# Kernel tuning notes

Hardware: AMD Instinct MI355X
Metric: run time of the kernel (lower is better)

## Reference

```python
import jax, jax.numpy as jnp
import numpy as np

HEADS = 4


def _forward(x_atoms, pos, edge_attr, molecular_features, emb_W, emb_b, mp_W1, mp_b1, mp_W2, mp_b2, ln_g, ln_b, attn_in_w, attn_in_b, attn_out_w, attn_out_b, pool_W, pool_b, mol_gate, lrn_gate, molemb_W1, molemb_b1, molemb_W2, molemb_b2, lrnemb_W1, lrnemb_b1, lrnemb_W2, lrnemb_b2, fus_W1, fus_b1, fus_W2, fus_b2, head_W1, head_b1, head_W2, head_b2, edge_index, batch_idx):
    N = x_atoms.shape[0]
    B = molecular_features.shape[0]
    A = N // B  # equal-size molecules; batch_idx = repeat(arange(B), A)
    H = emb_W.shape[1]
    L = mp_W1.shape[0]
    src, dst = edge_index[0], edge_index[1]  # PyG: x_j = x[src], x_i = x[dst]
    x = x_atoms @ emb_W + emb_b
    # distance features (constant across layers)
    diff = pos[dst] - pos[src]
    d = jnp.sqrt(jnp.sum(diff * diff, axis=1, keepdims=True) + 1e-12)
    dist_feat = jnp.concatenate([d, 1.0 / (1.0 + d), jnp.exp(-d)], axis=1)  # [E,3]
    ones_e = jnp.ones((src.shape[0], 1), x.dtype)
    cnt = jnp.maximum(jax.ops.segment_sum(ones_e, dst, num_segments=N), 1.0)
    for l in range(L):
        res = x
        msg = jnp.concatenate([x[dst], x[src], dist_feat], axis=1)  # [E, 2H+3]
        msg = jax.nn.relu(msg @ mp_W1[l] + mp_b1[l]) @ mp_W2[l] + mp_b2[l]
        x = jax.ops.segment_sum(msg, dst, num_segments=N) / cnt  # mean aggregation
        y = x + res
        mu = y.mean(-1, keepdims=True)
        var = jnp.var(y, axis=-1, keepdims=True)
        x = (y - mu) * jax.lax.rsqrt(var + 1e-5) * ln_g[l] + ln_b[l]
    xm = x.reshape(B, A, H)
    explicit = xm.mean(axis=1)  # scatter_mean over equal-size graphs
    # per-molecule multi-head self-attention (torch MHA, eval mode)
    hd = H // HEADS
    qkv = xm @ attn_in_w.T + attn_in_b
    q, k, v = jnp.split(qkv, 3, axis=-1)
    q = q.reshape(B, A, HEADS, hd)
    k = k.reshape(B, A, HEADS, hd)
    v = v.reshape(B, A, HEADS, hd)
    scores = jnp.einsum('bqhd,bkhd->bhqk', q, k) / jnp.sqrt(jnp.asarray(hd, x.dtype))
    att = jax.nn.softmax(scores, axis=-1)
    o = jnp.einsum('bhqk,bkhd->bqhd', att, v).reshape(B, A, H)
    attended = o @ attn_out_w.T + attn_out_b
    aw = jax.nn.softmax(jnp.sum(attended * xm, axis=-1), axis=1)  # [B,A]
    wmean = jnp.sum(attended * aw[..., None], axis=1)
    maxp = attended.max(axis=1)
    meanp = attended.mean(axis=1)
    stdp = jnp.std(attended, axis=1, ddof=1)  # torch.std unbiased
    pooled = jnp.stack([wmean, maxp, meanp, stdp], axis=0)  # [4,B,H]
    proj = jnp.einsum('kbh,khf->kbf', pooled, pool_W) + pool_b[:, None, :]
    learned = jnp.moveaxis(proj, 0, 1).reshape(B, -1)  # [B,LF]
    # per-property gated MLPs, vectorized over P (atom gates are computed but unused in the source)
    gm = molecular_features[None] * jax.nn.sigmoid(mol_gate)[:, None, :]
    gl = learned[None] * jax.nn.sigmoid(lrn_gate)[:, None, :]
    molrep = jax.nn.relu(jnp.einsum('pbm,pmh->pbh', gm, molemb_W1) + molemb_b1[:, None, :])
    molrep = jnp.einsum('pbh,phk->pbk', molrep, molemb_W2) + molemb_b2[:, None, :]
    lrnrep = jax.nn.relu(jnp.einsum('pbm,pmh->pbh', gl, lrnemb_W1) + lrnemb_b1[:, None, :])
    lrnrep = jnp.einsum('pbh,phk->pbk', lrnrep, lrnemb_W2) + lrnemb_b2[:, None, :]
    P = mol_gate.shape[0]
    comb = jnp.concatenate([jnp.broadcast_to(explicit[None], (P, B, H)), molrep, lrnrep], axis=-1)
    fused = jax.nn.relu(jnp.einsum('pbc,pch->pbh', comb, fus_W1) + fus_b1[:, None, :])
    fused = jnp.einsum('pbh,phk->pbk', fused, fus_W2) + fus_b2[:, None, :]
    h = jax.nn.relu(jnp.einsum('pbh,phk->pbk', fused, head_W1) + head_b1[:, None, :])
    out = jnp.einsum('pbk,pko->pbo', h, head_W2) + head_b2[:, None, :]
    return out  # [P,B,1]: stacked predictions for the 4 properties


def setup_inputs() -> dict:
    key = jax.random.key(0)
    ks = jax.random.split(key, 24)
    B, A, F, M, H, LF, L, P = 1024, 32, 64, 200, 128, 64, 3, 4
    N = B * A
    E = N * 16
    H2, H4, Q = H // 2, H // 4, LF // 4
    n = lambda i, shape, s=1.0: jax.random.normal(ks[i], shape, dtype=jnp.float32) * s
    inp = {}
    inp['x_atoms'] = n(0, (N, F))
    inp['pos'] = n(1, (N, 3)) * 3.0
    inp['edge_attr'] = n(2, (E, 4))
    inp['molecular_features'] = n(3, (B, M))
    inp['emb_W'] = n(4, (F, H), 0.1)
    inp['emb_b'] = jnp.zeros((H,), jnp.float32)
    inp['mp_W1'] = n(5, (L, 2 * H + 3, H), 0.05)
    inp['mp_b1'] = jnp.zeros((L, H), jnp.float32)
    inp['mp_W2'] = n(6, (L, H, H), 0.05)
    inp['mp_b2'] = jnp.zeros((L, H), jnp.float32)
    inp['ln_g'] = jnp.ones((L, H), jnp.float32)
    inp['ln_b'] = jnp.zeros((L, H), jnp.float32)
    inp['attn_in_w'] = n(7, (3 * H, H), 0.08)
    inp['attn_in_b'] = jnp.zeros((3 * H,), jnp.float32)
    inp['attn_out_w'] = n(8, (H, H), 0.08)
    inp['attn_out_b'] = jnp.zeros((H,), jnp.float32)
    inp['pool_W'] = n(9, (4, H, Q), 0.08)
    inp['pool_b'] = jnp.zeros((4, Q), jnp.float32)
    inp['mol_gate'] = n(10, (P, M))
    inp['lrn_gate'] = n(11, (P, LF))
    inp['molemb_W1'] = n(12, (P, M, H2), 0.08)
    inp['molemb_b1'] = jnp.zeros((P, H2), jnp.float32)
    inp['molemb_W2'] = n(13, (P, H2, H2), 0.08)
    inp['molemb_b2'] = jnp.zeros((P, H2), jnp.float32)
    inp['lrnemb_W1'] = n(14, (P, LF, H2), 0.08)
    inp['lrnemb_b1'] = jnp.zeros((P, H2), jnp.float32)
    inp['lrnemb_W2'] = n(15, (P, H2, H2), 0.08)
    inp['lrnemb_b2'] = jnp.zeros((P, H2), jnp.float32)
    inp['fus_W1'] = n(16, (P, 2 * H, H), 0.08)
    inp['fus_b1'] = jnp.zeros((P, H), jnp.float32)
    inp['fus_W2'] = n(17, (P, H, H2), 0.08)
    inp['fus_b2'] = jnp.zeros((P, H2), jnp.float32)
    inp['head_W1'] = n(18, (P, H2, H4), 0.08)
    inp['head_b1'] = jnp.zeros((P, H4), jnp.float32)
    inp['head_W2'] = n(19, (P, H4, 1), 0.08)
    inp['head_b2'] = jnp.zeros((P, 1), jnp.float32)
    inp['edge_index'] = jax.random.randint(ks[20], (2, E), 0, N)
    inp['batch_idx'] = jnp.repeat(jnp.arange(B), A)
    return inp


def reference(x_atoms, pos, edge_attr, molecular_features, emb_W, emb_b, mp_W1, mp_b1, mp_W2, mp_b2, ln_g, ln_b, attn_in_w, attn_in_b, attn_out_w, attn_out_b, pool_W, pool_b, mol_gate, lrn_gate, molemb_W1, molemb_b1, molemb_W2, molemb_b2, lrnemb_W1, lrnemb_b1, lrnemb_W2, lrnemb_b2, fus_W1, fus_b1, fus_W2, fus_b2, head_W1, head_b1, head_W2, head_b2, edge_index, batch_idx):
    return _forward(x_atoms, pos, edge_attr, molecular_features, emb_W, emb_b, mp_W1, mp_b1, mp_W2, mp_b2, ln_g, ln_b, attn_in_w, attn_in_b, attn_out_w, attn_out_b, pool_W, pool_b, mol_gate, lrn_gate, molemb_W1, molemb_b1, molemb_W2, molemb_b2, lrnemb_W1, lrnemb_b1, lrnemb_W2, lrnemb_b2, fus_W1, fus_b1, fus_W2, fus_b2, head_W1, head_b1, head_W2, head_b2, edge_index, batch_idx)
```

## Files before the change

### kernel.cpp

```cpp
#include <hip/hip_runtime.h>

#define NE 524288
#define NN 32768
#define NB 1024

#define F4(p) (*(const float4*)(p))

typedef __bf16 bf16x8 __attribute__((ext_vector_type(8)));
typedef float  f32x4  __attribute__((ext_vector_type(4)));

__device__ __forceinline__ float sigmoidf_(float v) { return 1.f / (1.f + expf(-v)); }

__device__ __forceinline__ void bf16split(float f, short &hi, short &lo) {
  unsigned u = __float_as_uint(f);
  unsigned rh = (u + 0x7FFFu + ((u >> 16) & 1u)) >> 16;
  float fh = __uint_as_float(rh << 16);
  float fl = f - fh;
  unsigned u2 = __float_as_uint(fl);
  unsigned rl = (u2 + 0x7FFFu + ((u2 >> 16) & 1u)) >> 16;
  hi = (short)rh; lo = (short)rl;
}

__device__ __forceinline__ void ld32(float* xr, const float* p) {
#pragma unroll
  for (int i = 0; i < 32; i += 4) {
    float4 v = F4(&p[i]);
    xr[i] = v.x; xr[i+1] = v.y; xr[i+2] = v.z; xr[i+3] = v.w;
  }
}

__device__ __forceinline__ float dot32r(const float* __restrict__ w, const float* xr) {
  float s = 0.f;
#pragma unroll
  for (int i = 0; i < 32; i += 4) {
    float4 ww = F4(&w[i]);
    s = fmaf(xr[i],   ww.x, s);
    s = fmaf(xr[i+1], ww.y, s);
    s = fmaf(xr[i+2], ww.z, s);
    s = fmaf(xr[i+3], ww.w, s);
  }
  return s;
}

__global__ __launch_bounds__(128) void embed_kernel(
    const float* __restrict__ xa, const float* __restrict__ W,
    const float* __restrict__ b, float* __restrict__ x)
{
  __shared__ float a[64];
  const int n = blockIdx.x, t = threadIdx.x;
  if (t < 64) a[t] = xa[n*64 + t];
  __syncthreads();
  float s = b[t];
#pragma unroll 8
  for (int f = 0; f < 64; ++f) s = fmaf(a[f], W[f*128 + t], s);
  x[n*128 + t] = s;
}

__global__ __launch_bounds__(256) void hist_kernel(const int* __restrict__ ei, int* __restrict__ cnt) {
  const int e = blockIdx.x*256 + threadIdx.x;
  atomicAdd(&cnt[ei[NE + e]], 1);
}

__global__ __launch_bounds__(1024) void scan_kernel(
    const int* __restrict__ cnt, int* __restrict__ off, int* __restrict__ cur)
{
  __shared__ int wsum[16];
  const int t = threadIdx.x;
  int local[32];
  const int base = t*32;
  int s = 0;
#pragma unroll
  for (int i = 0; i < 32; ++i) { local[i] = cnt[base+i]; s += local[i]; }
  int pre = s;
  const int lane = t & 63;
#pragma unroll
  for (int o = 1; o < 64; o <<= 1) { int v = __shfl_up(pre, o); if (lane >= o) pre += v; }
  if (lane == 63) wsum[t >> 6] = pre;
  __syncthreads();
  if (t == 0) { int a = 0; for (int w = 0; w < 16; ++w) { int v = wsum[w]; wsum[w] = a; a += v; } }
  __syncthreads();
  int excl = wsum[t >> 6] + pre - s;
#pragma unroll
  for (int i = 0; i < 32; ++i) { off[base+i] = excl; cur[base+i] = excl; excl += local[i]; }
  if (t == 1023) off[NN] = excl;
}

__global__ __launch_bounds__(256) void scatter_kernel(
    const float* __restrict__ pos, const int* __restrict__ ei,
    int* __restrict__ cur, int* __restrict__ csr_src, float* __restrict__ csr_df)
{
  const int e = blockIdx.x*256 + threadIdx.x;
  const int s = ei[e];
  const int d = ei[NE + e];
  float dx = pos[d*3+0] - pos[s*3+0];
  float dy = pos[d*3+1] - pos[s*3+1];
  float dz = pos[d*3+2] - pos[s*3+2];
  float dist = sqrtf(dx*dx + dy*dy + dz*dz + 1e-12f);
  const int slot = atomicAdd(&cur[d], 1);
  csr_src[slot] = s;
  csr_df[slot*3+0] = dist;
  csr_df[slot*3+1] = 1.f/(1.f + dist);
  csr_df[slot*3+2] = expf(-dist);
}

__device__ __forceinline__ void pack_decode(int r, int N, int &k, int &n) {
  const int j = r & 7, lane = (r >> 3) & 63, rest = r >> 9;
  const int NT = N >> 4;
  const int t = rest % NT, kc = rest / NT;
  k = kc*32 + (lane >> 4)*8 + j;
  n = t*16 + (lane & 15);
}

__global__ __launch_bounds__(256) void prep_kernel(
    const float* __restrict__ mp_W1, const float* __restrict__ mp_W2,
    const float* __restrict__ win, const float* __restrict__ wout,
    const float* __restrict__ mp_b1,
    short* __restrict__ bh, short* __restrict__ bl, float* __restrict__ pqbias)
{
  const int i = blockIdx.x*256 + threadIdx.x;
  if (i < 768) { const int l = i >> 8, t = i & 255; pqbias[i] = t < 128 ? mp_b1[l*128 + t] : 0.f; }
  if (i >= 212992) return;
  int k, n; float v;
  if (i < 98304) {
    const int l = i / 32768, r = i % 32768;
    pack_decode(r, 256, k, n);
    const float* W = mp_W1 + (size_t)l*259*128;
    v = (n < 128) ? W[k*128 + n] : W[(128+k)*128 + (n-128)];
  } else if (i < 147456) {
    const int q = i - 98304, l = q / 16384, r = q % 16384;
    pack_decode(r, 128, k, n);
    v = mp_W2[(size_t)l*16384 + k*128 + n];
  } else if (i < 196608) {
    const int r = i - 147456;
    pack_decode(r, 384, k, n);
    v = win[n*128 + k];
  } else {
    const int r = i - 196608;
    pack_decode(r, 128, k, n);
    v = wout[n*128 + k];
  }
  short h, lo; bf16split(v, h, lo);
  bh[i] = h; bl[i] = lo;
}

__global__ __launch_bounds__(256, 2) void mfma_gemm_kernel(
    const float* __restrict__ A, int lda,
    const short* __restrict__ Bh, const short* __restrict__ Bl,
    const float* __restrict__ bias, float* __restrict__ C, int ncols)
{
  const int lane = threadIdx.x & 63, wid = threadIdx.x >> 6;
  const int m0 = blockIdx.x * 128 + wid * 32;
  const int n0 = blockIdx.y * 64;
  const int NT = ncols >> 4;
  const int cl = lane & 15, kg = lane >> 4;

  bf16x8 Ah[2][4], Al[2][4];
#pragma unroll
  for (int s = 0; s < 2; ++s)
#pragma unroll
    for (int kc = 0; kc < 4; ++kc) {
      const float* ap = &A[(size_t)(m0 + s*16 + cl)*lda + kc*32 + kg*8];
      const float4 f0 = F4(ap), f1 = F4(ap + 4);
      const float fv[8] = {f0.x,f0.y,f0.z,f0.w,f1.x,f1.y,f1.z,f1.w};
      union { short s[8]; bf16x8 b; } uh, ul;
#pragma unroll
      for (int j = 0; j < 8; ++j) bf16split(fv[j], uh.s[j], ul.s[j]);
      Ah[s][kc] = uh.b; Al[s][kc] = ul.b;
    }

  f32x4 acc[2][4];
#pragma unroll
  for (int s = 0; s < 2; ++s)
#pragma unroll
    for (int t = 0; t < 4; ++t) acc[s][t] = (f32x4){0.f,0.f,0.f,0.f};

#pragma unroll
  for (int kc = 0; kc < 4; ++kc) {
    bf16x8 Bfh[4], Bfl[4];
#pragma unroll
    for (int t = 0; t < 4; ++t) {
      const size_t off = (((size_t)(kc*NT + (n0 >> 4) + t))*64 + lane)*8;
      Bfh[t] = *(const bf16x8*)&Bh[off];
      Bfl[t] = *(const bf16x8*)&Bl[off];
    }
#pragma unroll
    for (int s = 0; s < 2; ++s)
#pragma unroll
      for (int t = 0; t < 4; ++t)
        acc[s][t] = __builtin_amdgcn_mfma_f32_16x16x32_bf16(Ah[s][kc], Bfh[t], acc[s][t], 0, 0, 0);
#pragma unroll
    for (int s = 0; s < 2; ++s)
#pragma unroll
      for (int t = 0; t < 4; ++t)
        acc[s][t] = __builtin_amdgcn_mfma_f32_16x16x32_bf16(Ah[s][kc], Bfl[t], acc[s][t], 0, 0, 0);
#pragma unroll
    for (int s = 0; s < 2; ++s)
#pragma unroll
      for (int t = 0; t < 4; ++t)
        acc[s][t] = __builtin_amdgcn_mfma_f32_16x16x32_bf16(Al[s][kc], Bfh[t], acc[s][t], 0, 0, 0);
  }

#pragma unroll
  for (int t = 0; t < 4; ++t) {
    const int col = n0 + t*16 + cl;
    const float bv = bias[col];
#pragma unroll
    for (int s = 0; s < 2; ++s) {
      const int rbase = m0 + s*16 + kg*4;
#pragma unroll
      for (int r = 0; r < 4; ++r)
        C[(size_t)(rbase + r)*ncols + col] = acc[s][t][r] + bv;
    }
  }
}

__global__ __launch_bounds__(256, 2) void mfma_gemm_ln_kernel(
    const float* __restrict__ A, int lda,
    const short* __restrict__ Bh, const short* __restrict__ Bl,
    const float* __restrict__ b2, const int* __restrict__ csr_off,
    const float* __restrict__ g, const float* __restrict__ bb,
    float* __restrict__ x)
{
  const int lane = threadIdx.x & 63, wid = threadIdx.x >> 6;
  const int m0 = blockIdx.x * 64 + wid * 16;
  const int cl = lane & 15, kg = lane >> 4;

  bf16x8 Ah[4], Al[4];
#pragma unroll
  for (int kc = 0; kc < 4; ++kc) {
    const float* ap = &A[(size_t)(m0 + cl)*lda + kc*32 + kg*8];
    const float4 f0 = F4(ap), f1 = F4(ap + 4);
    const float fv[8] = {f0.x,f0.y,f0.z,f0.w,f1.x,f1.y,f1.z,f1.w};
    union { short s[8]; bf16x8 b; } uh, ul;
#pragma unroll
    for (int j = 0; j < 8; ++j) bf16split(fv[j], uh.s[j], ul.s[j]);
    Ah[kc] = uh.b; Al[kc] = ul.b;
  }

  f32x4 acc[8];
#pragma unroll
  for (int t = 0; t < 8; ++t) acc[t] = (f32x4){0.f,0.f,0.f,0.f};

#pragma unroll
  for (int kc = 0; kc < 4; ++kc) {
    bf16x8 Bfh[8], Bfl[8];
#pragma unroll
    for (int t = 0; t < 8; ++t) {
      const size_t off = (((size_t)(kc*8 + t))*64 + lane)*8;
      Bfh[t] = *(const bf16x8*)&Bh[off];
      Bfl[t] = *(const bf16x8*)&Bl[off];
    }
#pragma unroll
    for (int t = 0; t < 8; ++t)
      acc[t] = __builtin_amdgcn_mfma_f32_16x16x32_bf16(Ah[kc], Bfh[t], acc[t], 0, 0, 0);
#pragma unroll
    for (int t = 0; t < 8; ++t)
      acc[t] = __builtin_amdgcn_mfma_f32_16x16x32_bf16(Ah[kc], Bfl[t], acc[t], 0, 0, 0);
#pragma unroll
    for (int t = 0; t < 8; ++t)
      acc[t] = __builtin_amdgcn_mfma_f32_16x16x32_bf16(Al[kc], Bfh[t], acc[t], 0, 0, 0);
  }

  const int r0 = m0 + kg*4;
  float sflag[4];
#pragma unroll
  for (int r = 0; r < 4; ++r)
    sflag[r] = (csr_off[r0 + r + 1] > csr_off[r0 + r]) ? 1.f : 0.f;

  float ps[4] = {0.f,0.f,0.f,0.f}, pq[4] = {0.f,0.f,0.f,0.f};
  float yv[8][4];
#pragma unroll
  for (int t = 0; t < 8; ++t) {
    const int col = t*16 + cl;
    const float b2v = b2[col];
#pragma unroll
    for (int r = 0; r < 4; ++r) {
      const float y = acc[t][r] + sflag[r]*b2v + x[(size_t)(r0 + r)*128 + col];
      yv[t][r] = y;
      ps[r] += y;
      pq[r] = fmaf(y, y, pq[r]);
    }
  }
#pragma unroll
  for (int o = 1; o < 16; o <<= 1) {
#pragma unroll
    for (int r = 0; r < 4; ++r) { ps[r] += __shfl_xor(ps[r], o); pq[r] += __shfl_xor(pq[r], o); }
  }
#pragma unroll
  for (int r = 0; r < 4; ++r) {
    const float mu = ps[r] * (1.f/128.f);
    const float var = pq[r]*(1.f/128.f) - mu*mu;
    const float rstd = rsqrtf(var + 1e-5f);
#pragma unroll
    for (int t = 0; t < 8; ++t) {
      const int col = t*16 + cl;
      x[(size_t)(r0 + r)*128 + col] = (yv[t][r] - mu)*rstd*g[col] + bb[col];
    }
  }
}

__global__ __launch_bounds__(256) void agg_kernel(
    float* __restrict__ PQc,
    const int* __restrict__ csr_off, const int* __restrict__ csr_src,
    const float* __restrict__ csr_df, const float* __restrict__ W1)
{
  const int tid = threadIdx.x;
  const int node = blockIdx.x*4 + (tid >> 6);
  const int lane = tid & 63;
  const int c0 = lane*2;
  const int off0 = csr_off[node], off1 = csr_off[node+1];

  const float* __restrict__ w1c = W1 + 256*128;
  const float w00 = w1c[c0],       w01 = w1c[c0+1];
  const float w10 = w1c[128+c0],   w11 = w1c[128+c0+1];
  const float w20 = w1c[256+c0],   w21 = w1c[256+c0+1];
  const float2 p = *(const float2*)&PQc[(size_t)node*256 + c0];

  float a0 = 0.f, a1 = 0.f;
  int e = off0;
  for (; e + 4 <= off1; e += 4) {
#pragma unroll
    for (int j = 0; j < 4; ++j) {
      const int src = csr_src[e+j];
      const float d0 = csr_df[(e+j)*3+0];
      const float d1 = csr_df[(e+j)*3+1];
      const float d2 = csr_df[(e+j)*3+2];
      const float2 q = *(const float2*)&PQc[(size_t)src*256 + 128 + c0];
      float h0 = p.x + q.x;
      h0 = fmaf(d0, w00, h0); h0 = fmaf(d1, w10, h0); h0 = fmaf(d2, w20, h0);
      float h1 = p.y + q.y;
      h1 = fmaf(d0, w01, h1); h1 = fmaf(d1, w11, h1); h1 = fmaf(d2, w21, h1);
      a0 += fmaxf(h0, 0.f);
      a1 += fmaxf(h1, 0.f);
    }
  }
  for (; e < off1; ++e) {
    const int src = csr_src[e];
    const float d0 = csr_df[e*3+0];
    const float d1 = csr_df[e*3+1];
    const float d2 = csr_df[e*3+2];
    const float2 q = *(const float2*)&PQc[(size_t)src*256 + 128 + c0];
    float h0 = p.x + q.x;
    h0 = fmaf(d0, w00, h0); h0 = fmaf(d1, w10, h0); h0 = fmaf(d2, w20, h0);
    float h1 = p.y + q.y;
    h1 = fmaf(d0, w01, h1); h1 = fmaf(d1, w11, h1); h1 = fmaf(d2, w21, h1);
    a0 += fmaxf(h0, 0.f);
    a1 += fmaxf(h1, 0.f);
  }
  const int deg = off1 - off0;
  const float rc = deg > 0 ? 1.f/(float)deg : 1.f;
  *(float2*)&PQc[(size_t)node*256 + c0] = make_float2(a0*rc, a1*rc);
}

__global__ __launch_bounds__(128) void attn_kernel(float* __restrict__ dqkv)
{
  __shared__ float sk[32*132];
  __shared__ float sv[32*132];
  const int tid = threadIdx.x;
  const int b = blockIdx.x;

  for (int idx = tid; idx < 1024; idx += 128) {
    const int a = idx >> 5, c4 = idx & 31;
    *(float4*)&sk[a*132 + c4*4] = F4(&dqkv[(size_t)(b*32+a)*384 + 128 + c4*4]);
    *(float4*)&sv[a*132 + c4*4] = F4(&dqkv[(size_t)(b*32+a)*384 + 256 + c4*4]);
  }
  __syncthreads();

  const int h = tid >> 5, qr = tid & 31;
  float qreg[32];
  ld32(qreg, &dqkv[(size_t)(b*32+qr)*384 + h*32]);

  float sc[32];
#pragma unroll
  for (int k = 0; k < 32; ++k)
    sc[k] = dot32r(&sk[k*132 + h*32], qreg) * 0.17677669529663687f;
  float mx = sc[0];
#pragma unroll
  for (int k = 1; k < 32; ++k) mx = fmaxf(mx, sc[k]);
  float se = 0.f;
#pragma unroll
  for (int k = 0; k < 32; ++k) { sc[k] = expf(sc[k] - mx); se += sc[k]; }
  const float inv = 1.f / se;

  __syncthreads();

  float od[32];
#pragma unroll
  for (int i = 0; i < 32; ++i) od[i] = 0.f;
#pragma unroll 4
  for (int k = 0; k < 32; ++k) {
    const float w = sc[k] * inv;
    const float* vr = &sv[k*132 + h*32];
#pragma unroll
    for (int i = 0; i < 32; i += 4) {
      float4 v = F4(&vr[i]);
      od[i]   = fmaf(w, v.x, od[i]);
      od[i+1] = fmaf(w, v.y, od[i+1]);
      od[i+2] = fmaf(w, v.z, od[i+2]);
      od[i+3] = fmaf(w, v.w, od[i+3]);
    }
  }
#pragma unroll
  for (int i = 0; i < 32; i += 4)
    *(float4*)&sk[qr*132 + h*32 + i] = make_float4(od[i], od[i+1], od[i+2], od[i+3]);
  __syncthreads();

  for (int idx = tid; idx < 1024; idx += 128) {
    const int a = idx >> 5, c4 = idx & 31;
    *(float4*)&dqkv[(size_t)(b*32+a)*384 + 256 + c4*4] = F4(&sk[a*132 + c4*4]);
  }
}

__global__ __launch_bounds__(128) void pool_kernel(
    const float* __restrict__ att, const float* __restrict__ x,
    const float* __restrict__ pW, const float* __restrict__ pb,
    float* __restrict__ expl, float* __restrict__ lrn)
{
  __shared__ float satt[32*132];
  __shared__ float sx[32*132];
  __shared__ float aw_l[32];
  __shared__ float spool[512];
  const int tid = threadIdx.x;
  const int b = blockIdx.x;

  for (int idx = tid; idx < 1024; idx += 128) {
    const int a = idx >> 5, c4 = idx & 31;
    *(float4*)&satt[a*132 + c4*4] = F4(&att[(size_t)(b*32+a)*128 + c4*4]);
    *(float4*)&sx[a*132 + c4*4]   = F4(&x[(size_t)(b*32+a)*128 + c4*4]);
  }
  __syncthreads();

  {
    const int a = tid >> 2, q4 = tid & 3;
    float sp = 0.f;
#pragma unroll
    for (int i = 0; i < 32; ++i)
      sp = fmaf(satt[a*132 + q4*32 + i], sx[a*132 + q4*32 + i], sp);
    sp += __shfl_xor(sp, 1);
    sp += __shfl_xor(sp, 2);
    if (q4 == 0) aw_l[a] = sp;
  }
  __syncthreads();

  {
    float awr[32];
    float mxl = aw_l[0];
#pragma unroll
    for (int a = 1; a < 32; ++a) mxl = fmaxf(mxl, aw_l[a]);
    float se = 0.f;
#pragma unroll
    for (int a = 0; a < 32; ++a) { awr[a] = expf(aw_l[a] - mxl); se += awr[a]; }
    const float inv = 1.f / se;
    const int c = tid;
    float mx = -3.4e38f, sm = 0.f, wm = 0.f, ex = 0.f;
#pragma unroll
    for (int a = 0; a < 32; ++a) {
      const float v = satt[a*132 + c];
      mx = fmaxf(mx, v);
      sm += v;
      wm = fmaf(v, awr[a], wm);
      ex += sx[a*132 + c];
    }
    wm *= inv;
    const float mean = sm * 0.03125f;
    float s2 = 0.f;
#pragma unroll
    for (int a = 0; a < 32; ++a) {
      const float d = satt[a*132 + c] - mean;
      s2 = fmaf(d, d, s2);
    }
    const float stdp = sqrtf(s2 * (1.f/31.f));
    expl[b*128 + c] = ex * 0.03125f;
    spool[c]       = wm;
    spool[128 + c] = mx;
    spool[256 + c] = mean;
    spool[384 + c] = stdp;
  }
  __syncthreads();

  if (tid < 64) {
    const int k = tid >> 4, qq = tid & 15;
    const float* pk = pW + k*2048;
    float s = pb[k*16 + qq];
    for (int h2 = 0; h2 < 128; ++h2)
      s = fmaf(spool[k*128 + h2], pk[h2*16 + qq], s);
    lrn[b*64 + tid] = s;
  }
}

__global__ __launch_bounds__(64) void head_kernel(
    const float* __restrict__ molf, const float* __restrict__ lrn,
    const float* __restrict__ expl,
    const float* __restrict__ mol_gate, const float* __restrict__ lrn_gate,
    const float* __restrict__ meW1, const float* __restrict__ meb1,
    const float* __restrict__ meW2, const float* __restrict__ meb2,
    const float* __restrict__ leW1, const float* __restrict__ leb1,
    const float* __restrict__ leW2, const float* __restrict__ leb2,
    const float* __restrict__ fW1, const float* __restrict__ fb1,
    const float* __restrict__ fW2, const float* __restrict__ fb2,
    const float* __restrict__ hW1, const float* __restrict__ hb1,
    const float* __restrict__ hW2, const float* __restrict__ hb2,
    float* __restrict__ out)
{
  const int b = blockIdx.x, p = blockIdx.y, t = threadIdx.x;
  __shared__ float sgm[200];
  __shared__ float sgl[64];
  __shared__ float sA[64];
  __shared__ float sB[64];
  __shared__ float scomb[256];
  __shared__ float sf1[128];
  __shared__ float sf2[64];

  for (int m = t; m < 200; m += 64)
    sgm[m] = molf[b*200 + m] * sigmoidf_(mol_gate[p*200 + m]);
  sgl[t] = lrn[b*64 + t] * sigmoidf_(lrn_gate[p*64 + t]);
  scomb[t]      = expl[b*128 + t];
  scomb[64 + t] = expl[b*128 + 64 + t];
  __syncthreads();

  {
    float s = meb1[p*64 + t];
    const float* w = meW1 + p*12800;
    for (int m = 0; m < 200; ++m) s = fmaf(sgm[m], w[m*64 + t], s);
    sA[t] = fmaxf(s, 0.f);
    float s2 = leb1[p*64 + t];
    const float* w2 = leW1 + p*4096;
#pragma unroll 8
    for (int m = 0; m < 64; ++m) s2 = fmaf(sgl[m], w2[m*64 + t], s2);
    sB[t] = fmaxf(s2, 0.f);
  }
  __syncthreads();
  {
    float s = meb2[p*64 + t];
    const float* w = meW2 + p*4096;
#pragma unroll 8
    for (int h = 0; h < 64; ++h) s = fmaf(sA[h], w[h*64 + t], s);
    scomb[128 + t] = s;
    float s2 = leb2[p*64 + t];
    const float* w2 = leW2 + p*4096;
#pragma unroll 8
    for (int h = 0; h < 64; ++h) s2 = fmaf(sB[h], w2[h*64 + t], s2);
    scomb[192 + t] = s2;
  }
  __syncthreads();
  {
    const float* w = fW1 + p*32768;
    float s0 = fb1[p*128 + t], s1 = fb1[p*128 + 64 + t];
    for (int c = 0; c < 256; ++c) {
      const float v = scomb[c];
      s0 = fmaf(v, w[c*128 + t], s0);
      s1 = fmaf(v, w[c*128 + 64 + t], s1);
    }
    sf1[t]      = fmaxf(s0, 0.f);
    sf1[64 + t] = fmaxf(s1, 0.f);
  }
  __syncthreads();
  {
    float s = fb2[p*64 + t];
    const float* w = fW2 + p*8192;
    for (int h = 0; h < 128; ++h) s = fmaf(sf1[h], w[h*64 + t], s);
    sf2[t] = s;
  }
  __syncthreads();
  float val = 0.f;
  if (t < 32) {
    float s = hb1[p*32 + t];
    const float* w = hW1 + p*2048;
#pragma unroll 8
    for (int h = 0; h < 64; ++h) s = fmaf(sf2[h], w[h*32 + t], s);
    val = fmaxf(s, 0.f) * hW2[p*32 + t];
  }
#pragma unroll
  for (int o = 1; o < 32; o <<= 1) val += __shfl_xor(val, o);
  if (t == 0) out[p*1024 + b] = val + hb2[p];
}

extern "C" void kernel_launch(void* const* d_in, const int* in_sizes, int n_in,
                              void* d_out, int out_size, void* d_ws, size_t ws_size,
                              hipStream_t stream) {
  const float* x_atoms    = (const float*)d_in[0];
  const float* pos        = (const float*)d_in[1];
  const float* molf       = (const float*)d_in[3];
  const float* emb_W      = (const float*)d_in[4];
  const float* emb_b      = (const float*)d_in[5];
  const float* mp_W1      = (const float*)d_in[6];
  const float* mp_b1      = (const float*)d_in[7];
  const float* mp_W2      = (const float*)d_in[8];
  const float* mp_b2      = (const float*)d_in[9];
  const float* ln_g       = (const float*)d_in[10];
  const float* ln_b       = (const float*)d_in[11];
  const float* attn_in_w  = (const float*)d_in[12];
  const float* attn_in_b  = (const float*)d_in[13];
  const float* attn_out_w = (const float*)d_in[14];
  const float* attn_out_b = (const float*)d_in[15];
  const float* pool_W     = (const float*)d_in[16];
  const float* pool_b     = (const float*)d_in[17];
  const float* mol_gate   = (const float*)d_in[18];
  const float* lrn_gate   = (const float*)d_in[19];
  const float* meW1       = (const float*)d_in[20];
  const float* meb1       = (const float*)d_in[21];
  const float* meW2       = (const float*)d_in[22];
  const float* meb2       = (const float*)d_in[23];
  const float* leW1       = (const float*)d_in[24];
  const float* leb1       = (const float*)d_in[25];
  const float* leW2       = (const float*)d_in[26];
  const float* leb2       = (const float*)d_in[27];
  const float* fW1        = (const float*)d_in[28];
  const float* fb1        = (const float*)d_in[29];
  const float* fW2        = (const float*)d_in[30];
  const float* fb2        = (const float*)d_in[31];
  const float* hW1        = (const float*)d_in[32];
  const float* hb1        = (const float*)d_in[33];
  const float* hW2        = (const float*)d_in[34];
  const float* hb2        = (const float*)d_in[35];
  const int*   ei         = (const int*)d_in[36];

  float* ws      = (float*)d_ws;
  float* x       = ws;
  float* PQc     = x + (size_t)NN*128;
  float* dqkv    = PQc;
  float* att     = PQc + (size_t)NN*384;
  float* csr_df  = att + (size_t)NN*128;
  int*   csr_src = (int*)(csr_df + (size_t)NE*3);
  int*   cnt_i   = csr_src + NE;
  int*   csr_off = cnt_i + NN;
  int*   cur     = csr_off + NN + 1;
  float* lrn     = (float*)(cur + NN);
  float* expl    = lrn + NB*64;
  float* pqbias  = expl + NB*128;
  short* bh      = (short*)(pqbias + 768);
  short* bl      = bh + 212992;

  const int W1AB_OFF = 0;
  const int W2_OFF   = 98304;
  const int WIN_OFF  = 147456;
  const int WOUT_OFF = 196608;

  hipMemsetAsync(cnt_i, 0, (size_t)NN*sizeof(int), stream);

  embed_kernel<<<NN, 128, 0, stream>>>(x_atoms, emb_W, emb_b, x);
  hist_kernel<<<NE/256, 256, 0, stream>>>(ei, cnt_i);
  scan_kernel<<<1, 1024, 0, stream>>>(cnt_i, csr_off, cur);
  scatter_kernel<<<NE/256, 256, 0, stream>>>(pos, ei, cur, csr_src, csr_df);
  prep_kernel<<<(212992 + 255)/256, 256, 0, stream>>>(mp_W1, mp_W2, attn_in_w, attn_out_w,
                                                      mp_b1, bh, bl, pqbias);

  for (int l = 0; l < 3; ++l) {
    mfma_gemm_kernel<<<dim3(NN/128, 4), 256, 0, stream>>>(
        x, 128, bh + W1AB_OFF + l*32768, bl + W1AB_OFF + l*32768,
        pqbias + l*256, PQc, 256);
    agg_kernel<<<NN/4, 256, 0, stream>>>(PQc, csr_off, csr_src, csr_df,
                                         mp_W1 + (size_t)l*259*128);
    mfma_gemm_ln_kernel<<<NN/64, 256, 0, stream>>>(
        PQc, 256, bh + W2_OFF + l*16384, bl + W2_OFF + l*16384,
        mp_b2 + l*128, csr_off, ln_g + l*128, ln_b + l*128, x);
  }

  mfma_gemm_kernel<<<dim3(NN/128, 6), 256, 0, stream>>>(
      x, 128, bh + WIN_OFF, bl + WIN_OFF, attn_in_b, dqkv, 384);
  attn_kernel<<<NB, 128, 0, stream>>>(dqkv);
  mfma_gemm_kernel<<<dim3(NN/128, 2), 256, 0, stream>>>(
      dqkv + 256, 384, bh + WOUT_OFF, bl + WOUT_OFF, attn_out_b, att, 128);
  pool_kernel<<<NB, 128, 0, stream>>>(att, x, pool_W, pool_b, expl, lrn);
  head_kernel<<<dim3(NB, 4), 64, 0, stream>>>(molf, lrn, expl, mol_gate, lrn_gate,
      meW1, meb1, meW2, meb2, leW1, leb1, leW2, leb2,
      fW1, fb1, fW2, fb2, hW1, hb1, hW2, hb2, (float*)d_out);
}
```

Baseline: 449.3 us.

## Store gathered Q half in bf16, widen agg gather batching, split reduction chains

```diff
diff --git a/kernel.cpp b/kernel.cpp
--- a/kernel.cpp
+++ b/kernel.cpp
@@ -19,6 +19,14 @@
   unsigned u2 = __float_as_uint(fl);
   unsigned rl = (u2 + 0x7FFFu + ((u2 >> 16) & 1u)) >> 16;
   hi = (short)rh; lo = (short)rl;
+}
+
+__device__ __forceinline__ unsigned short f2bf(float f) {
+  unsigned u = __float_as_uint(f);
+  return (unsigned short)((u + 0x7FFFu + ((u >> 16) & 1u)) >> 16);
+}
+__device__ __forceinline__ float bf2f(unsigned short h) {
+  return __uint_as_float(((unsigned)h) << 16);
 }
 
 __device__ __forceinline__ void ld32(float* xr, const float* p) {
@@ -146,7 +154,8 @@
 __global__ __launch_bounds__(256, 2) void mfma_gemm_kernel(
     const float* __restrict__ A, int lda,
     const short* __restrict__ Bh, const short* __restrict__ Bl,
-    const float* __restrict__ bias, float* __restrict__ C, int ncols)
+    const float* __restrict__ bias, float* __restrict__ C, int ncols, int ldc,
+    unsigned short* __restrict__ qbf)
 {
   const int lane = threadIdx.x & 63, wid = threadIdx.x >> 6;
   const int m0 = blockIdx.x * 128 + wid * 32;
@@ -208,8 +217,13 @@
     for (int s = 0; s < 2; ++s) {
       const int rbase = m0 + s*16 + kg*4;
 #pragma unroll
-      for (int r = 0; r < 4; ++r)
-        C[(size_t)(rbase + r)*ncols + col] = acc[s][t][r] + bv;
+      for (int r = 0; r < 4; ++r) {
+        const float v = acc[s][t][r] + bv;
+        if (qbf && col >= 128)
+          qbf[(size_t)(rbase + r)*128 + (col - 128)] = f2bf(v);
+        else
+          C[(size_t)(rbase + r)*ldc + col] = v;
+      }
     }
   }
 }
@@ -299,8 +313,8 @@
   }
 }
 
-__global__ __launch_bounds__(256) void agg_kernel(
-    float* __restrict__ PQc,
+__global__ __launch_bounds__(256, 6) void agg_kernel(
+    float* __restrict__ P, const unsigned short* __restrict__ Qbf,
     const int* __restrict__ csr_off, const int* __restrict__ csr_src,
     const float* __restrict__ csr_df, const float* __restrict__ W1)
 {
@@ -314,42 +328,47 @@
   const float w00 = w1c[c0],       w01 = w1c[c0+1];
   const float w10 = w1c[128+c0],   w11 = w1c[128+c0+1];
   const float w20 = w1c[256+c0],   w21 = w1c[256+c0+1];
-  const float2 p = *(const float2*)&PQc[(size_t)node*256 + c0];
+  const float2 p = *(const float2*)&P[(size_t)node*128 + c0];
 
   float a0 = 0.f, a1 = 0.f;
   int e = off0;
-  for (; e + 4 <= off1; e += 4) {
-#pragma unroll
-    for (int j = 0; j < 4; ++j) {
-      const int src = csr_src[e+j];
-      const float d0 = csr_df[(e+j)*3+0];
-      const float d1 = csr_df[(e+j)*3+1];
-      const float d2 = csr_df[(e+j)*3+2];
-      const float2 q = *(const float2*)&PQc[(size_t)src*256 + 128 + c0];
-      float h0 = p.x + q.x;
-      h0 = fmaf(d0, w00, h0); h0 = fmaf(d1, w10, h0); h0 = fmaf(d2, w20, h0);
-      float h1 = p.y + q.y;
-      h1 = fmaf(d0, w01, h1); h1 = fmaf(d1, w11, h1); h1 = fmaf(d2, w21, h1);
+  for (; e + 8 <= off1; e += 8) {
+    int sr[8];
+#pragma unroll
+    for (int j = 0; j < 8; ++j) sr[j] = csr_src[e+j];
+    ushort2 qv[8];
+#pragma unroll
+    for (int j = 0; j < 8; ++j) qv[j] = *(const ushort2*)&Qbf[(size_t)sr[j]*128 + c0];
+    float dfv[8][3];
+#pragma unroll
+    for (int j = 0; j < 8; ++j) {
+      dfv[j][0] = csr_df[(e+j)*3+0];
+      dfv[j][1] = csr_df[(e+j)*3+1];
+      dfv[j][2] = csr_df[(e+j)*3+2];
+    }
+#pragma unroll
+    for (int j = 0; j < 8; ++j) {
+      float h0 = p.x + bf2f(qv[j].x);
+      h0 = fmaf(dfv[j][0], w00, h0); h0 = fmaf(dfv[j][1], w10, h0); h0 = fmaf(dfv[j][2], w20, h0);
+      float h1 = p.y + bf2f(qv[j].y);
+      h1 = fmaf(dfv[j][0], w01, h1); h1 = fmaf(dfv[j][1], w11, h1); h1 = fmaf(dfv[j][2], w21, h1);
       a0 += fmaxf(h0, 0.f);
       a1 += fmaxf(h1, 0.f);
     }
   }
   for (; e < off1; ++e) {
-    const int src = csr_src[e];
-    const float d0 = csr_df[e*3+0];
-    const float d1 = csr_df[e*3+1];
-    const float d2 = csr_df[e*3+2];
-    const float2 q = *(const float2*)&PQc[(size_t)src*256 + 128 + c0];
-    float h0 = p.x + q.x;
+    const ushort2 qv = *(const ushort2*)&Qbf[(size_t)csr_src[e]*128 + c0];
+    const float d0 = csr_df[e*3+0], d1 = csr_df[e*3+1], d2 = csr_df[e*3+2];
+    float h0 = p.x + bf2f(qv.x);
     h0 = fmaf(d0, w00, h0); h0 = fmaf(d1, w10, h0); h0 = fmaf(d2, w20, h0);
-    float h1 = p.y + q.y;
+    float h1 = p.y + bf2f(qv.y);
     h1 = fmaf(d0, w01, h1); h1 = fmaf(d1, w11, h1); h1 = fmaf(d2, w21, h1);
     a0 += fmaxf(h0, 0.f);
     a1 += fmaxf(h1, 0.f);
   }
   const int deg = off1 - off0;
   const float rc = deg > 0 ? 1.f/(float)deg : 1.f;
-  *(float2*)&PQc[(size_t)node*256 + c0] = make_float2(a0*rc, a1*rc);
+  *(float2*)&P[(size_t)node*128 + c0] = make_float2(a0*rc, a1*rc);
 }
 
 __global__ __launch_bounds__(128) void attn_kernel(float* __restrict__ dqkv)
@@ -481,10 +500,14 @@
   if (tid < 64) {
     const int k = tid >> 4, qq = tid & 15;
     const float* pk = pW + k*2048;
-    float s = pb[k*16 + qq];
-    for (int h2 = 0; h2 < 128; ++h2)
-      s = fmaf(spool[k*128 + h2], pk[h2*16 + qq], s);
-    lrn[b*64 + tid] = s;
+    float s0 = 0.f, s1 = 0.f, s2 = 0.f, s3 = 0.f;
+    for (int h2 = 0; h2 < 128; h2 += 4) {
+      s0 = fmaf(spool[k*128 + h2],   pk[h2*16 + qq],     s0);
+      s1 = fmaf(spool[k*128 + h2+1], pk[(h2+1)*16 + qq], s1);
+      s2 = fmaf(spool[k*128 + h2+2], pk[(h2+2)*16 + qq], s2);
+      s3 = fmaf(spool[k*128 + h2+3], pk[(h2+3)*16 + qq], s3);
+    }
+    lrn[b*64 + tid] = pb[k*16 + qq] + (s0+s1) + (s2+s3);
   }
 }
 
@@ -519,56 +542,89 @@
   __syncthreads();
 
   {
-    float s = meb1[p*64 + t];
     const float* w = meW1 + p*12800;
-    for (int m = 0; m < 200; ++m) s = fmaf(sgm[m], w[m*64 + t], s);
-    sA[t] = fmaxf(s, 0.f);
-    float s2 = leb1[p*64 + t];
+    float a0=0.f,a1=0.f,a2=0.f,a3=0.f;
+    for (int m = 0; m < 200; m += 4) {
+      a0 = fmaf(sgm[m],   w[m*64 + t],       a0);
+      a1 = fmaf(sgm[m+1], w[(m+1)*64 + t],   a1);
+      a2 = fmaf(sgm[m+2], w[(m+2)*64 + t],   a2);
+      a3 = fmaf(sgm[m+3], w[(m+3)*64 + t],   a3);
+    }
+    sA[t] = fmaxf(meb1[p*64 + t] + (a0+a1) + (a2+a3), 0.f);
     const float* w2 = leW1 + p*4096;
-#pragma unroll 8
-    for (int m = 0; m < 64; ++m) s2 = fmaf(sgl[m], w2[m*64 + t], s2);
-    sB[t] = fmaxf(s2, 0.f);
+    float b0=0.f,b1_=0.f,b2_=0.f,b3=0.f;
+    for (int m = 0; m < 64; m += 4) {
+      b0  = fmaf(sgl[m],   w2[m*64 + t],     b0);
+      b1_ = fmaf(sgl[m+1], w2[(m+1)*64 + t], b1_);
+      b2_ = fmaf(sgl[m+2], w2[(m+2)*64 + t], b2_);
+      b3  = fmaf(sgl[m+3], w2[(m+3)*64 + t], b3);
+    }
+    sB[t] = fmaxf(leb1[p*64 + t] + (b0+b1_) + (b2_+b3), 0.f);
   }
   __syncthreads();
   {
-    float s = meb2[p*64 + t];
     const float* w = meW2 + p*4096;
-#pragma unroll 8
-    for (int h = 0; h < 64; ++h) s = fmaf(sA[h], w[h*64 + t], s);
-    scomb[128 + t] = s;
-    float s2 = leb2[p*64 + t];
+    float a0=0.f,a1=0.f,a2=0.f,a3=0.f;
+    for (int h = 0; h < 64; h += 4) {
+      a0 = fmaf(sA[h],   w[h*64 + t],       a0);
+      a1 = fmaf(sA[h+1], w[(h+1)*64 + t],   a1);
+      a2 = fmaf(sA[h+2], w[(h+2)*64 + t],   a2);
+      a3 = fmaf(sA[h+3], w[(h+3)*64 + t],   a3);
+    }
+    scomb[128 + t] = meb2[p*64 + t] + (a0+a1) + (a2+a3);
     const float* w2 = leW2 + p*4096;
-#pragma unroll 8
-    for (int h = 0; h < 64; ++h) s2 = fmaf(sB[h], w2[h*64 + t], s2);
-    scomb[192 + t] = s2;
+    float b0=0.f,b1_=0.f,b2_=0.f,b3=0.f;
+    for (int h = 0; h < 64; h += 4) {
+      b0  = fmaf(sB[h],   w2[h*64 + t],     b0);
+      b1_ = fmaf(sB[h+1], w2[(h+1)*64 + t], b1_);
+      b2_ = fmaf(sB[h+2], w2[(h+2)*64 + t], b2_);
+      b3  = fmaf(sB[h+3], w2[(h+3)*64 + t], b3);
+    }
+    scomb[192 + t] = leb2[p*64 + t] + (b0+b1_) + (b2_+b3);
   }
   __syncthreads();
   {
     const float* w = fW1 + p*32768;
-    float s0 = fb1[p*128 + t], s1 = fb1[p*128 + 64 + t];
-    for (int c = 0; c < 256; ++c) {
-      const float v = scomb[c];
-      s0 = fmaf(v, w[c*128 + t], s0);
-      s1 = fmaf(v, w[c*128 + 64 + t], s1);
-    }
-    sf1[t]      = fmaxf(s0, 0.f);
-    sf1[64 + t] = fmaxf(s1, 0.f);
+    float s00=0.f,s01=0.f,s02=0.f,s03=0.f;
+    float s10=0.f,s11=0.f,s12=0.f,s13=0.f;
+    for (int c = 0; c < 256; c += 4) {
+      const float v0 = scomb[c], v1 = scomb[c+1], v2 = scomb[c+2], v3 = scomb[c+3];
+      s00 = fmaf(v0, w[c*128 + t],          s00);
+      s01 = fmaf(v1, w[(c+1)*128 + t],      s01);
+      s02 = fmaf(v2, w[(c+2)*128 + t],      s02);
+      s03 = fmaf(v3, w[(c+3)*128 + t],      s03);
+      s10 = fmaf(v0, w[c*128 + 64 + t],     s10);
+      s11 = fmaf(v1, w[(c+1)*128 + 64 + t], s11);
+      s12 = fmaf(v2, w[(c+2)*128 + 64 + t], s12);
+      s13 = fmaf(v3, w[(c+3)*128 + 64 + t], s13);
+    }
+    sf1[t]      = fmaxf(fb1[p*128 + t]      + (s00+s01) + (s02+s03), 0.f);
+    sf1[64 + t] = fmaxf(fb1[p*128 + 64 + t] + (s10+s11) + (s12+s13), 0.f);
   }
   __syncthreads();
   {
-    float s = fb2[p*64 + t];
     const float* w = fW2 + p*8192;
-    for (int h = 0; h < 128; ++h) s = fmaf(sf1[h], w[h*64 + t], s);
-    sf2[t] = s;
+    float a0=0.f,a1=0.f,a2=0.f,a3=0.f;
+    for (int h = 0; h < 128; h += 4) {
+      a0 = fmaf(sf1[h],   w[h*64 + t],       a0);
+      a1 = fmaf(sf1[h+1], w[(h+1)*64 + t],   a1);
+      a2 = fmaf(sf1[h+2], w[(h+2)*64 + t],   a2);
+      a3 = fmaf(sf1[h+3], w[(h+3)*64 + t],   a3);
+    }
+    sf2[t] = fb2[p*64 + t] + (a0+a1) + (a2+a3);
   }
   __syncthreads();
   float val = 0.f;
   if (t < 32) {
-    float s = hb1[p*32 + t];
     const float* w = hW1 + p*2048;
-#pragma unroll 8
-    for (int h = 0; h < 64; ++h) s = fmaf(sf2[h], w[h*32 + t], s);
-    val = fmaxf(s, 0.f) * hW2[p*32 + t];
+    float a0=0.f,a1=0.f,a2=0.f,a3=0.f;
+    for (int h = 0; h < 64; h += 4) {
+      a0 = fmaf(sf2[h],   w[h*32 + t],       a0);
+      a1 = fmaf(sf2[h+1], w[(h+1)*32 + t],   a1);
+      a2 = fmaf(sf2[h+2], w[(h+2)*32 + t],   a2);
+      a3 = fmaf(sf2[h+3], w[(h+3)*32 + t],   a3);
+    }
+    val = fmaxf(hb1[p*32 + t] + (a0+a1) + (a2+a3), 0.f) * hW2[p*32 + t];
   }
 #pragma unroll
   for (int o = 1; o < 32; o <<= 1) val += __shfl_xor(val, o);
@@ -617,9 +673,11 @@
 
   float* ws      = (float*)d_ws;
   float* x       = ws;
-  float* PQc     = x + (size_t)NN*128;
-  float* dqkv    = PQc;
-  float* att     = PQc + (size_t)NN*384;
+  float* region  = x + (size_t)NN*128;
+  float* P       = region;
+  unsigned short* Qbf = (unsigned short*)(region + (size_t)NN*128);
+  float* dqkv    = region;
+  float* att     = region + (size_t)NN*384;
   float* csr_df  = att + (size_t)NN*128;
   int*   csr_src = (int*)(csr_df + (size_t)NE*3);
   int*   cnt_i   = csr_src + NE;
@@ -648,19 +706,19 @@
   for (int l = 0; l < 3; ++l) {
     mfma_gemm_kernel<<<dim3(NN/128, 4), 256, 0, stream>>>(
         x, 128, bh + W1AB_OFF + l*32768, bl + W1AB_OFF + l*32768,
-        pqbias + l*256, PQc, 256);
-    agg_kernel<<<NN/4, 256, 0, stream>>>(PQc, csr_off, csr_src, csr_df,
+        pqbias + l*256, P, 256, 128, Qbf);
+    agg_kernel<<<NN/4, 256, 0, stream>>>(P, Qbf, csr_off, csr_src, csr_df,
                                          mp_W1 + (size_t)l*259*128);
     mfma_gemm_ln_kernel<<<NN/64, 256, 0, stream>>>(
-        PQc, 256, bh + W2_OFF + l*16384, bl + W2_OFF + l*16384,
+        P, 128, bh + W2_OFF + l*16384, bl + W2_OFF + l*16384,
         mp_b2 + l*128, csr_off, ln_g + l*128, ln_b + l*128, x);
   }
 
   mfma_gemm_kernel<<<dim3(NN/128, 6), 256, 0, stream>>>(
-      x, 128, bh + WIN_OFF, bl + WIN_OFF, attn_in_b, dqkv, 384);
+      x, 128, bh + WIN_OFF, bl + WIN_OFF, attn_in_b, dqkv, 384, 384, nullptr);
   attn_kernel<<<NB, 128, 0, stream>>>(dqkv);
   mfma_gemm_kernel<<<dim3(NN/128, 2), 256, 0, stream>>>(
-      dqkv + 256, 384, bh + WOUT_OFF, bl + WOUT_OFF, attn_out_b, att, 128);
+      dqkv + 256, 384, bh + WOUT_OFF, bl + WOUT_OFF, attn_out_b, att, 128, 128, nullptr);
   pool_kernel<<<NB, 128, 0, stream>>>(att, x, pool_W, pool_b, expl, lrn);
   head_kernel<<<dim3(NB, 4), 64, 0, stream>>>(molf, lrn, expl, mol_gate, lrn_gate,
       meW1, meb1, meW2, meb2, leW1, leb1, leW2, leb2,
```

New measurement: 429.0 us. 1.05x faster.
